# Performance work log

Measured on AMD Instinct MI355X. Metric: run time of the kernel, lower is better.

## Reference

```python
import jax, jax.numpy as jnp
import numpy as np

NUM_USERS = 100000
NUM_ITEMS = 50000
EMBED_DIM = 64
N_LAYERS = 3
SOCIAL_LAYERS = 2
NNZ_R = 3200000
NNZ_S = 2000000


def setup_inputs() -> dict:
    key = jax.random.key(0)
    ks = jax.random.split(key, 8)
    return {
        "user_emb": jax.random.normal(ks[0], (NUM_USERS, EMBED_DIM), jnp.float32) * 0.1,
        "item_emb": jax.random.normal(ks[1], (NUM_ITEMS, EMBED_DIM), jnp.float32) * 0.1,
        "r_vals": jax.random.uniform(ks[2], (NNZ_R,), jnp.float32) * 0.01,
        "s_vals": jax.random.uniform(ks[3], (NNZ_S,), jnp.float32) * 0.01,
        "r_rows": jax.random.randint(ks[4], (NNZ_R,), 0, NUM_USERS),
        "r_cols": jax.random.randint(ks[5], (NNZ_R,), 0, NUM_ITEMS),
        "s_rows": jax.random.randint(ks[6], (NNZ_S,), 0, NUM_USERS),
        "s_cols": jax.random.randint(ks[7], (NNZ_S,), 0, NUM_USERS),
    }


def spmm(rows, cols, vals, x, n_rows):
    # sparse(COO) @ dense: out[r] += v * x[c]
    return jax.ops.segment_sum(vals[:, None] * x[cols], rows, num_segments=n_rows)


def l2_normalize(x, eps=1e-12):
    return x / jnp.maximum(jnp.linalg.norm(x, axis=1, keepdims=True), eps)


def reference(user_emb, item_emb, r_vals, s_vals, r_rows, r_cols, s_rows, s_cols):
    # LightGCN-style propagation over user-item bipartite graph
    u, i = user_emb, item_emb
    u_sum, i_sum = user_emb, item_emb
    for _ in range(N_LAYERS):
        u_next = spmm(r_rows, r_cols, r_vals, i, NUM_USERS)   # R @ item
        i_next = spmm(r_cols, r_rows, r_vals, u, NUM_ITEMS)   # R^T @ user
        u, i = u_next, i_next  # dropout = identity in eval mode
        u_sum = u_sum + u
        i_sum = i_sum + i
    user_final = u_sum / (N_LAYERS + 1)
    item_final = i_sum / (N_LAYERS + 1)

    # social graph propagation on user embeddings
    s = user_emb
    s_sum = user_emb
    for _ in range(SOCIAL_LAYERS):
        s = spmm(s_rows, s_cols, s_vals, s, NUM_USERS)
        s_sum = s_sum + s
    social_final = s_sum / (SOCIAL_LAYERS + 1)

    final_user = l2_normalize(0.6 * user_final + 0.4 * social_final)
    final_item = l2_normalize(item_final)
    return final_user, final_item
```

## Files before the change

kernel.cpp:

```cpp
#include <hip/hip_runtime.h>

constexpr int NUM_USERS = 100000;
constexpr int NUM_ITEMS = 50000;
constexpr int DIM = 64;
constexpr int NNZ_R = 3200000;
constexpr int NNZ_S = 2000000;
constexpr int NNZ_TOT = NNZ_R + NNZ_R + NNZ_S;

constexpr int BSH_U = 8, BROWS_U = 256;
constexpr int BSH_I = 7, BROWS_I = 128;
constexpr int NC_U = (NUM_USERS + BROWS_U - 1) / BROWS_U;
constexpr int NC_I = (NUM_ITEMS + BROWS_I - 1) / BROWS_I;
constexpr int NC_S = NC_U;
constexpr int NC = NC_U + NC_I + NC_S;
constexpr int NBLK = 256;
constexpr int NPB = NBLK * NC;
constexpr int CHUNK_R = NNZ_R / NBLK;
constexpr int CHUNK_S = (NNZ_S + NBLK - 1) / NBLK;

__device__ __forceinline__ float bf2f(unsigned short u) {
    return __uint_as_float((unsigned)u << 16);
}
__device__ __forceinline__ unsigned short f2bf(float f) {
    unsigned u = __float_as_uint(f);
    return (unsigned short)((u + 0x7FFFu + ((u >> 16) & 1u)) >> 16);
}
__device__ __forceinline__ float bflo(unsigned r) { return __uint_as_float(r << 16); }
__device__ __forceinline__ float bfhi(unsigned r) { return __uint_as_float(r & 0xFFFF0000u); }

__global__ __launch_bounds__(1024) void hist_lds(const int* __restrict__ rr,
                                                 const int* __restrict__ rc,
                                                 const int* __restrict__ sr,
                                                 int* __restrict__ cntPB ) {
    __shared__ int lds[NC];
    int k = blockIdx.x, tid = threadIdx.x;
    for (int c = tid; c < NC; c += 1024) lds[c] = 0;
    __syncthreads();
    int r0 = k * CHUNK_R, r1 = r0 + CHUNK_R;
    int s0 = k * CHUNK_S, s1 = min(s0 + CHUNK_S, NNZ_S);
    for (int i = r0 + tid; i < r1; i += 1024) {
        atomicAdd(&lds[rr[i] >> BSH_U], 1);
        atomicAdd(&lds[NC_U + (rc[i] >> BSH_I)], 1);
    }
    for (int i = s0 + tid; i < s1; i += 1024)
        atomicAdd(&lds[NC_U + NC_I + (sr[i] >> BSH_U)], 1);
    __syncthreads();
    for (int c = tid; c < NC; c += 1024) cntPB[c * NBLK + k] = lds[c];
}

__global__ __launch_bounds__(NBLK) void scan_bkt(int* __restrict__ cntPB,
                                                 int* __restrict__ bktTot) {
    int c = blockIdx.x, t = threadIdx.x;
    __shared__ int sh[NBLK];
    int v = cntPB[c * NBLK + t];
    sh[t] = v;
    __syncthreads();
    for (int off = 1; off < NBLK; off <<= 1) {
        int u = (t >= off) ? sh[t - off] : 0;
        __syncthreads();
        sh[t] += u;
        __syncthreads();
    }
    cntPB[c * NBLK + t] = sh[t] - v;
    if (t == NBLK - 1) bktTot[c] = sh[t];
}

__global__ __launch_bounds__(1024) void scan_top(int* __restrict__ B ) {
    __shared__ int part[1024];
    int t = threadIdx.x;
    const int chunk = (NC + 1023) >> 10;
    int lo = t * chunk, hi = min(lo + chunk, NC);
    int s = 0;
    for (int i = lo; i < hi; ++i) s += B[i];
    part[t] = s;
    __syncthreads();
    for (int off = 1; off < 1024; off <<= 1) {
        int v = (t >= off) ? part[t - off] : 0;
        __syncthreads();
        part[t] += v;
        __syncthreads();
    }
    int excl = (t == 0) ? 0 : part[t - 1];
    for (int i = lo; i < hi; ++i) {
        int v = B[i];
        B[i] = excl;
        excl += v;
    }
    if (t == 1023) B[NC] = part[1023];
}

__global__ __launch_bounds__(1024) void bin_pass(const int* __restrict__ rr,
                                                 const int* __restrict__ rc,
                                                 const float* __restrict__ rv,
                                                 const int* __restrict__ sr,
                                                 const int* __restrict__ sc,
                                                 const float* __restrict__ sv,
                                                 const int* __restrict__ cntPB,
                                                 const int* __restrict__ bktBase,
                                                 int2* __restrict__ ent) {
    __shared__ int lds[NC];
    int k = blockIdx.x, tid = threadIdx.x;
    for (int c = tid; c < NC; c += 1024)
        lds[c] = bktBase[c] + cntPB[c * NBLK + k];
    __syncthreads();
    int r0 = k * CHUNK_R, r1 = r0 + CHUNK_R;
    int s0 = k * CHUNK_S, s1 = min(s0 + CHUNK_S, NNZ_S);
    for (int i = r0 + tid; i < r1; i += 1024) {
        int r = rr[i], c = rc[i];
        int v = __float_as_int(rv[i]);
        int pu = atomicAdd(&lds[r >> BSH_U], 1);
        ent[pu] = make_int2(((r & (BROWS_U - 1)) << 17) | c, v);
        int pi = atomicAdd(&lds[NC_U + (c >> BSH_I)], 1);
        ent[pi] = make_int2(((c & (BROWS_I - 1)) << 17) | r, v);
    }
    for (int i = s0 + tid; i < s1; i += 1024) {
        int r = sr[i];
        int ps = atomicAdd(&lds[NC_U + NC_I + (r >> BSH_U)], 1);
        ent[ps] = make_int2(((r & (BROWS_U - 1)) << 17) | sc[i], __float_as_int(sv[i]));
    }
}

__global__ __launch_bounds__(512) void sort_buckets(const int2* __restrict__ src,
                                                    int2* __restrict__ dst,
                                                    const int* __restrict__ bktBase,
                                                    int* __restrict__ rPu,
                                                    int* __restrict__ rPi,
                                                    int* __restrict__ rPs) {
    int gb = blockIdx.x;
    int* rowptr;
    int brows, lb, nrows;
    if (gb < NC_U)              { rowptr = rPu; brows = BROWS_U; lb = gb;               nrows = NUM_USERS; }
    else if (gb < NC_U + NC_I)  { rowptr = rPi; brows = BROWS_I; lb = gb - NC_U;        nrows = NUM_ITEMS; }
    else                        { rowptr = rPs; brows = BROWS_U; lb = gb - NC_U - NC_I; nrows = NUM_USERS; }
    int t = threadIdx.x;
    __shared__ int cnt[256];
    __shared__ int part[256];
    __shared__ int ofs[256];
    if (t < 256) cnt[t] = 0;
    __syncthreads();
    int b0 = bktBase[gb], b1 = bktBase[gb + 1];
    for (int i = b0 + t; i < b1; i += 512)
        atomicAdd(&cnt[(unsigned)src[i].x >> 17], 1);
    __syncthreads();
    if (t < 256) part[t] = cnt[t];
    __syncthreads();
    for (int off = 1; off < 256; off <<= 1) {
        int v = 0;
        if (t < 256 && t >= off) v = part[t - off];
        __syncthreads();
        if (t < 256) part[t] += v;
        __syncthreads();
    }
    if (t < 256) ofs[t] = part[t] - cnt[t];
    __syncthreads();
    int gr = lb * brows + t;
    if (t < brows && gr < nrows) rowptr[gr] = b0 + ofs[t];
    if (gb == 0 && t == 0) {
        rPu[NUM_USERS] = NNZ_R;
        rPi[NUM_ITEMS] = 2 * NNZ_R;
        rPs[NUM_USERS] = NNZ_TOT;
    }
    __syncthreads();
    for (int i = b0 + t; i < b1; i += 512) {
        int2 v = src[i];
        int lr = (unsigned)v.x >> 17;
        int pos = b0 + atomicAdd(&ofs[lr], 1);
        dst[pos] = make_int2(v.x & 0x1FFFF, v.y);
    }
}

struct SpmmOp {
    const int* rowptr;
    const int2* ent;
    const unsigned short* x;
    unsigned short* out;
    float* acc;
    float w;
    int nrows;
};

__global__ __launch_bounds__(256, 4) void spmm2(SpmmOp A, SpmmOp B, int ablocks) {
    bool isA = (int)blockIdx.x < ablocks;
    SpmmOp op = isA ? A : B;
    int bid = isA ? blockIdx.x : blockIdx.x - ablocks;
    int row = bid * 4 + (threadIdx.x >> 6);
    if (row >= op.nrows) return;
    int lane = threadIdx.x & 63;
    int g = lane >> 4;
    int q = lane & 15;
    const int2* __restrict__ ent = op.ent;
    const unsigned short* __restrict__ x = op.x;
    int e = op.rowptr[row], end = op.rowptr[row + 1];
    float s0 = 0.f, s1 = 0.f, s2 = 0.f, s3 = 0.f;
    for (; e + 16 <= end; e += 16) {
        int2 n0 = ent[e + g];
        int2 n1 = ent[e + 4 + g];
        int2 n2 = ent[e + 8 + g];
        int2 n3 = ent[e + 12 + g];
        uint2 r0 = *reinterpret_cast<const uint2*>(x + (size_t)n0.x * DIM + q * 4);
        uint2 r1 = *reinterpret_cast<const uint2*>(x + (size_t)n1.x * DIM + q * 4);
        uint2 r2 = *reinterpret_cast<const uint2*>(x + (size_t)n2.x * DIM + q * 4);
        uint2 r3 = *reinterpret_cast<const uint2*>(x + (size_t)n3.x * DIM + q * 4);
        float v0 = __int_as_float(n0.y), v1 = __int_as_float(n1.y);
        float v2 = __int_as_float(n2.y), v3 = __int_as_float(n3.y);
        s0 += v0 * bflo(r0.x); s1 += v0 * bfhi(r0.x); s2 += v0 * bflo(r0.y); s3 += v0 * bfhi(r0.y);
        s0 += v1 * bflo(r1.x); s1 += v1 * bfhi(r1.x); s2 += v1 * bflo(r1.y); s3 += v1 * bfhi(r1.y);
        s0 += v2 * bflo(r2.x); s1 += v2 * bfhi(r2.x); s2 += v2 * bflo(r2.y); s3 += v2 * bfhi(r2.y);
        s0 += v3 * bflo(r3.x); s1 += v3 * bfhi(r3.x); s2 += v3 * bflo(r3.y); s3 += v3 * bfhi(r3.y);
    }
    for (; e < end; e += 4) {
        if (e + g < end) {
            int2 n = ent[e + g];
            uint2 r = *reinterpret_cast<const uint2*>(x + (size_t)n.x * DIM + q * 4);
            float v = __int_as_float(n.y);
            s0 += v * bflo(r.x); s1 += v * bfhi(r.x);
            s2 += v * bflo(r.y); s3 += v * bfhi(r.y);
        }
    }
    s0 += __shfl_xor(s0, 16, 64); s0 += __shfl_xor(s0, 32, 64);
    s1 += __shfl_xor(s1, 16, 64); s1 += __shfl_xor(s1, 32, 64);
    s2 += __shfl_xor(s2, 16, 64); s2 += __shfl_xor(s2, 32, 64);
    s3 += __shfl_xor(s3, 16, 64); s3 += __shfl_xor(s3, 32, 64);
    if (g == 0) {
        size_t base = (size_t)row * DIM + q * 4;
        if (op.out) {
            uint2 o;
            o.x = (unsigned)f2bf(s0) | ((unsigned)f2bf(s1) << 16);
            o.y = (unsigned)f2bf(s2) | ((unsigned)f2bf(s3) << 16);
            *reinterpret_cast<uint2*>(op.out + base) = o;
        }
        float4* a = reinterpret_cast<float4*>(op.acc + base);
        float4 av = *a;
        av.x += op.w * s0; av.y += op.w * s1; av.z += op.w * s2; av.w += op.w * s3;
        *a = av;
    }
}

__global__ void init_acc(const float* __restrict__ ue, const float* __restrict__ ie,
                         float* __restrict__ accU, float* __restrict__ accI,
                         unsigned short* __restrict__ ueB, unsigned short* __restrict__ ieB,
                         int u4, int i4) {
    const float wu = 0.6f / 4.0f + 0.4f / 3.0f;
    const float wi = 0.25f;
    int i = blockIdx.x * blockDim.x + threadIdx.x;
    int st = gridDim.x * blockDim.x;
    int n4 = u4 + i4;
    for (; i < n4; i += st) {
        if (i < u4) {
            float4 v = reinterpret_cast<const float4*>(ue)[i];
            reinterpret_cast<float4*>(accU)[i] = make_float4(wu * v.x, wu * v.y, wu * v.z, wu * v.w);
            ushort4 b;
            b.x = f2bf(v.x); b.y = f2bf(v.y); b.z = f2bf(v.z); b.w = f2bf(v.w);
            reinterpret_cast<ushort4*>(ueB)[i] = b;
        } else {
            int j = i - u4;
            float4 v = reinterpret_cast<const float4*>(ie)[j];
            reinterpret_cast<float4*>(accI)[j] = make_float4(wi * v.x, wi * v.y, wi * v.z, wi * v.w);
            ushort4 b;
            b.x = f2bf(v.x); b.y = f2bf(v.y); b.z = f2bf(v.z); b.w = f2bf(v.w);
            reinterpret_cast<ushort4*>(ieB)[j] = b;
        }
    }
}

__global__ void finalize_kernel(float* __restrict__ out, int nrows) {
    int row = blockIdx.x * 4 + (threadIdx.x >> 6);
    if (row >= nrows) return;
    int d = threadIdx.x & 63;
    int idx = row * DIM + d;
    float val = out[idx];
    float sq = val * val;
    #pragma unroll
    for (int off = 32; off; off >>= 1) sq += __shfl_xor(sq, off, 64);
    out[idx] = val / fmaxf(sqrtf(sq), 1e-12f);
}

extern "C" void kernel_launch(void* const* d_in, const int* in_sizes, int n_in,
                              void* d_out, int out_size, void* d_ws, size_t ws_size,
                              hipStream_t stream) {
    const float* user_emb = (const float*)d_in[0];
    const float* item_emb = (const float*)d_in[1];
    const float* r_vals   = (const float*)d_in[2];
    const float* s_vals   = (const float*)d_in[3];
    const int*   r_rows   = (const int*)d_in[4];
    const int*   r_cols   = (const int*)d_in[5];
    const int*   s_rows   = (const int*)d_in[6];
    const int*   s_cols   = (const int*)d_in[7];

    const size_t U = (size_t)NUM_USERS * DIM;
    const size_t I = (size_t)NUM_ITEMS * DIM;

    int2* ent_sorted = (int2*)d_ws;
    char* region2 = (char*)(ent_sorted + NNZ_TOT);
    int2* ent_bin = (int2*)region2;
    unsigned short* ueB = (unsigned short*)region2;
    unsigned short* ieB = ueB + U;
    unsigned short* uA  = ieB + I;
    unsigned short* uB  = uA + U;
    unsigned short* iA  = uB + U;
    unsigned short* iB  = iA + I;
    int* cntPB   = (int*)(region2 + (size_t)NNZ_TOT * 8);
    int* bktBase = cntPB + NPB;
    int* rPu = bktBase + NC + 1;
    int* rPi = rPu + NUM_USERS + 1;
    int* rPs = rPi + NUM_ITEMS + 1;

    float* accU = (float*)d_out;
    float* accI = (float*)d_out + U;

    dim3 blk(256);

    hist_lds<<<NBLK, 1024, 0, stream>>>(r_rows, r_cols, s_rows, cntPB);
    scan_bkt<<<NC, NBLK, 0, stream>>>(cntPB, bktBase);
    scan_top<<<1, 1024, 0, stream>>>(bktBase);
    bin_pass<<<NBLK, 1024, 0, stream>>>(r_rows, r_cols, r_vals, s_rows, s_cols, s_vals,
                                        cntPB, bktBase, ent_bin);
    sort_buckets<<<NC, 512, 0, stream>>>(ent_bin, ent_sorted, bktBase, rPu, rPi, rPs);

    init_acc<<<2048, blk, 0, stream>>>(user_emb, item_emb, accU, accI, ueB, ieB,
                                       (int)(U / 4), (int)(I / 4));

    const float WU = 0.6f / 4.0f, WI = 0.25f, WS = 0.4f / 3.0f;
    int ub = (NUM_USERS + 3) / 4, ib = (NUM_ITEMS + 3) / 4;

    SpmmOp u1{rPu, ent_sorted, ieB, uA, accU, WU, NUM_USERS};
    SpmmOp i1{rPi, ent_sorted, ueB, iA, accI, WI, NUM_ITEMS};
    spmm2<<<ub + ib, blk, 0, stream>>>(u1, i1, ub);

    SpmmOp u2{rPu, ent_sorted, iA, uB, accU, WU, NUM_USERS};
    SpmmOp i2{rPi, ent_sorted, uA, iB, accI, WI, NUM_ITEMS};
    spmm2<<<ub + ib, blk, 0, stream>>>(u2, i2, ub);

    SpmmOp u3{rPu, ent_sorted, iB, nullptr, accU, WU, NUM_USERS};
    SpmmOp i3{rPi, ent_sorted, uB, nullptr, accI, WI, NUM_ITEMS};
    spmm2<<<ub + ib, blk, 0, stream>>>(u3, i3, ub);

    SpmmOp so1{rPs, ent_sorted, ueB, uA, accU, WS, NUM_USERS};
    spmm2<<<ub, blk, 0, stream>>>(so1, so1, ub);
    SpmmOp so2{rPs, ent_sorted, uA, nullptr, accU, WS, NUM_USERS};
    spmm2<<<ub, blk, 0, stream>>>(so2, so2, ub);

    finalize_kernel<<<(NUM_USERS + NUM_ITEMS + 3) / 4, blk, 0, stream>>>(
        (float*)d_out, NUM_USERS + NUM_ITEMS);
}
```

Baseline: 705.5 us.

## Stage bin_pass scatter through LDS local counting sort for coalesced writes

Rewrites the binning scatter to process edges in superblocks. For each superblock it counts bucket sizes in LDS, runs a block-wide prefix scan, places entries into an LDS staging buffer grouped by bucket, and then writes them to global memory in bucket order. The goal is to turn scattered 8-byte global writes into short contiguous runs per bucket. The cost is extra passes over the input per superblock, many block barriers for the scan, and a large LDS footprint that limits occupancy to one block per CU.

```diff
diff --git a/kernel.cpp b/kernel.cpp
--- a/kernel.cpp
+++ b/kernel.cpp
@@ -18,6 +18,9 @@
 constexpr int CHUNK_R = NNZ_R / NBLK;
 constexpr int CHUNK_S = (NNZ_S + NBLK - 1) / NBLK;
 
+constexpr int SB_EDGES = 4096;
+constexpr int SB_PAIRS = 8192;
+
 __device__ __forceinline__ float bf2f(unsigned short u) {
     return __uint_as_float((unsigned)u << 16);
 }
@@ -98,25 +101,102 @@
                                                  const int* __restrict__ cntPB,
                                                  const int* __restrict__ bktBase,
                                                  int2* __restrict__ ent) {
-    __shared__ int lds[NC];
+    __shared__ int cur[NC];
+    __shared__ int cnt[NC];
+    __shared__ int lstart[NC];
+    __shared__ int lcur[NC];
+    __shared__ int part[1024];
+    __shared__ int2 stage[SB_PAIRS];
+    __shared__ int gaddr[SB_PAIRS];
     int k = blockIdx.x, tid = threadIdx.x;
     for (int c = tid; c < NC; c += 1024)
-        lds[c] = bktBase[c] + cntPB[c * NBLK + k];
-    __syncthreads();
-    int r0 = k * CHUNK_R, r1 = r0 + CHUNK_R;
-    int s0 = k * CHUNK_S, s1 = min(s0 + CHUNK_S, NNZ_S);
-    for (int i = r0 + tid; i < r1; i += 1024) {
-        int r = rr[i], c = rc[i];
-        int v = __float_as_int(rv[i]);
-        int pu = atomicAdd(&lds[r >> BSH_U], 1);
-        ent[pu] = make_int2(((r & (BROWS_U - 1)) << 17) | c, v);
-        int pi = atomicAdd(&lds[NC_U + (c >> BSH_I)], 1);
-        ent[pi] = make_int2(((c & (BROWS_I - 1)) << 17) | r, v);
-    }
-    for (int i = s0 + tid; i < s1; i += 1024) {
-        int r = sr[i];
-        int ps = atomicAdd(&lds[NC_U + NC_I + (r >> BSH_U)], 1);
-        ent[ps] = make_int2(((r & (BROWS_U - 1)) << 17) | sc[i], __float_as_int(sv[i]));
+        cur[c] = bktBase[c] + cntPB[c * NBLK + k];
+
+    int r0 = k * CHUNK_R;
+    for (int sb = 0; sb < CHUNK_R; sb += SB_EDGES) {
+        int nE = min(SB_EDGES, CHUNK_R - sb);
+        int base = r0 + sb;
+        for (int c = tid; c < NC; c += 1024) { cnt[c] = 0; lcur[c] = 0; }
+        __syncthreads();
+        for (int i = tid; i < nE; i += 1024) {
+            atomicAdd(&cnt[rr[base + i] >> BSH_U], 1);
+            atomicAdd(&cnt[NC_U + (rc[base + i] >> BSH_I)], 1);
+        }
+        __syncthreads();
+        int o0 = 2 * tid, o1 = 2 * tid + 1;
+        int a = (o0 < NC) ? cnt[o0] : 0;
+        int b = (o1 < NC) ? cnt[o1] : 0;
+        part[tid] = a + b;
+        __syncthreads();
+        for (int off = 1; off < 1024; off <<= 1) {
+            int v = (tid >= off) ? part[tid - off] : 0;
+            __syncthreads();
+            part[tid] += v;
+            __syncthreads();
+        }
+        int ex = (tid == 0) ? 0 : part[tid - 1];
+        if (o0 < NC) lstart[o0] = ex;
+        if (o1 < NC) lstart[o1] = ex + a;
+        __syncthreads();
+        for (int i = tid; i < nE; i += 1024) {
+            int r = rr[base + i], c = rc[base + i];
+            int v = __float_as_int(rv[base + i]);
+            int cu_ = r >> BSH_U;
+            int j = atomicAdd(&lcur[cu_], 1);
+            int lp = lstart[cu_] + j;
+            stage[lp] = make_int2(((r & (BROWS_U - 1)) << 17) | c, v);
+            gaddr[lp] = cur[cu_] + j;
+            int ci_ = NC_U + (c >> BSH_I);
+            int j2 = atomicAdd(&lcur[ci_], 1);
+            int lp2 = lstart[ci_] + j2;
+            stage[lp2] = make_int2(((c & (BROWS_I - 1)) << 17) | r, v);
+            gaddr[lp2] = cur[ci_] + j2;
+        }
+        __syncthreads();
+        int nP = 2 * nE;
+        for (int s = tid; s < nP; s += 1024)
+            ent[gaddr[s]] = stage[s];
+        for (int c = tid; c < NC; c += 1024) cur[c] += cnt[c];
+        __syncthreads();
+    }
+
+    int s0 = k * CHUNK_S, sEnd = min(s0 + CHUNK_S, NNZ_S);
+    for (int sb = s0; sb < sEnd; sb += SB_PAIRS) {
+        int nE = min(SB_PAIRS, sEnd - sb);
+        for (int c = tid; c < NC; c += 1024) { cnt[c] = 0; lcur[c] = 0; }
+        __syncthreads();
+        for (int i = tid; i < nE; i += 1024)
+            atomicAdd(&cnt[NC_U + NC_I + (sr[sb + i] >> BSH_U)], 1);
+        __syncthreads();
+        int o0 = 2 * tid, o1 = 2 * tid + 1;
+        int a = (o0 < NC) ? cnt[o0] : 0;
+        int b = (o1 < NC) ? cnt[o1] : 0;
+        part[tid] = a + b;
+        __syncthreads();
+        for (int off = 1; off < 1024; off <<= 1) {
+            int v = (tid >= off) ? part[tid - off] : 0;
+            __syncthreads();
+            part[tid] += v;
+            __syncthreads();
+        }
+        int ex = (tid == 0) ? 0 : part[tid - 1];
+        if (o0 < NC) lstart[o0] = ex;
+        if (o1 < NC) lstart[o1] = ex + a;
+        __syncthreads();
+        for (int i = tid; i < nE; i += 1024) {
+            int r = sr[sb + i];
+            int cs_ = NC_U + NC_I + (r >> BSH_U);
+            int j = atomicAdd(&lcur[cs_], 1);
+            int lp = lstart[cs_] + j;
+            stage[lp] = make_int2(((r & (BROWS_U - 1)) << 17) | sc[sb + i],
+                                  __float_as_int(sv[sb + i]));
+            gaddr[lp] = cur[cs_] + j;
+        }
+        __syncthreads();
+        for (int s = tid; s < nE; s += 1024)
+            ent[gaddr[s]] = stage[s];
+        for (int c = tid; c < NC; c += 1024) cur[c] += cnt[c];
+        __syncthreads();
     }
 }
 
```

Result: faster. 648.4 us (-8.1%).
